# Kernel optimization log

Measured on AMD Instinct MI355X. Metric: run time of the kernel, lower is better.

## Reference

```python
import jax, jax.numpy as jnp
import numpy as np

N = 50000          # nodes
E = 1600000        # edges (avg degree 32)
B = 64             # graphs in batch
D_NODE = 128
D_EDGE = 64
D_EMB = 128
D_HID = 2 * D_EMB  # GCN output channels
EPS = 1e-5


def setup_inputs() -> dict:
    key = jax.random.key(0)
    ks = jax.random.split(key, 12)
    g = lambda k, shape: jax.random.normal(k, shape, jnp.float32) * (shape[0] ** -0.5)
    return {
        "x": jax.random.normal(ks[0], (N, D_NODE), jnp.float32),
        "edge_attr": jax.random.normal(ks[1], (E, D_EDGE), jnp.float32),
        "edge_index": jax.random.randint(ks[2], (2, E), 0, N),
        "batch": jnp.sort(jax.random.randint(ks[3], (N,), 0, B)),
        # GCNConv params
        "W1": g(ks[4], (D_NODE, D_HID)), "b1": jnp.zeros((D_HID,), jnp.float32),
        # TransformerConv params (heads=1)
        "Wq": g(ks[5], (D_HID, D_EMB)), "bq": jnp.zeros((D_EMB,), jnp.float32),
        "Wk": g(ks[6], (D_HID, D_EMB)), "bk": jnp.zeros((D_EMB,), jnp.float32),
        "Wv": g(ks[7], (D_HID, D_EMB)), "bv": jnp.zeros((D_EMB,), jnp.float32),
        "We": g(ks[8], (D_EDGE, D_EMB)), "be": jnp.zeros((D_EMB,), jnp.float32),
        "Wr": g(ks[9], (D_HID, D_EMB)), "br": jnp.zeros((D_EMB,), jnp.float32),
        # LayerNorm params
        "gamma": jnp.ones((D_EMB,), jnp.float32), "beta": jnp.zeros((D_EMB,), jnp.float32),
    }


def _forward(x, edge_attr, edge_index, batch,
             W1, b1, Wq, bq, Wk, bk, Wv, bv, We, be, Wr, br, gamma, beta):
    src, dst = edge_index[0], edge_index[1]

    # ---- GCNConv: symmetric normalization with self-loops ----
    xw = x @ W1                                                # [N, D_HID]
    deg = 1.0 + jax.ops.segment_sum(jnp.ones((E,), x.dtype), dst, num_segments=N)
    dinv = jax.lax.rsqrt(deg)                                  # deg >= 1
    norm = dinv[src] * dinv[dst]                               # [E]
    agg = jax.ops.segment_sum(xw[src] * norm[:, None], dst, num_segments=N)
    h = agg + xw * (dinv * dinv)[:, None] + b1                 # self-loop term
    h = jax.nn.relu(h)                                         # dropout = identity (eval)

    # ---- TransformerConv (heads=1, edge_dim) ----
    q = h @ Wq + bq                                            # [N, D_EMB]
    k = h @ Wk + bk
    v = h @ Wv + bv
    e = edge_attr @ We + be                                    # [E, D_EMB]
    k_j = k[src] + e
    v_j = v[src] + e
    logits = jnp.sum(q[dst] * k_j, axis=-1) / jnp.sqrt(jnp.float32(D_EMB))  # [E]
    # segment softmax over incoming edges of each target node
    lmax = jax.ops.segment_max(logits, dst, num_segments=N)
    exp_l = jnp.exp(logits - lmax[dst])
    denom = jax.ops.segment_sum(exp_l, dst, num_segments=N)
    alpha = exp_l / denom[dst]                                 # [E]
    out = jax.ops.segment_sum(alpha[:, None] * v_j, dst, num_segments=N)
    out = out + h @ Wr + br                                    # root/skip connection

    # ---- LayerNorm + ReLU ----
    mu = jnp.mean(out, axis=-1, keepdims=True)
    var = jnp.var(out, axis=-1, keepdims=True)
    out = (out - mu) * jax.lax.rsqrt(var + EPS) * gamma + beta
    out = jax.nn.relu(out)

    # ---- global mean pool over graphs ----
    sums = jax.ops.segment_sum(out, batch, num_segments=B)     # [B, D_EMB]
    cnts = jax.ops.segment_sum(jnp.ones((N,), out.dtype), batch, num_segments=B)
    return sums / jnp.maximum(cnts, 1.0)[:, None]


def reference(x, edge_attr, edge_index, batch,
              W1, b1, Wq, bq, Wk, bk, Wv, bv, We, be, Wr, br, gamma, beta):
    return _forward(x, edge_attr, edge_index, batch,
                    W1, b1, Wq, bq, Wk, bk, Wv, bv, We, be, Wr, br, gamma, beta)
```

## Files before the change

### kernel.cpp

```cpp
#include <hip/hip_runtime.h>

typedef short bf16x8 __attribute__((ext_vector_type(8)));
typedef float f32x4 __attribute__((ext_vector_type(4)));

#define DN 128
#define DE 64
#define DEMB 128
#define DHID 256
#define SCALE 0.08838834764831845f

__device__ __forceinline__ ushort f2bf(float f) {
  unsigned u = __float_as_uint(f);
  return (ushort)((u + 0x7FFFu + ((u >> 16) & 1u)) >> 16);
}
__device__ __forceinline__ float bf2f(ushort u) {
  return __uint_as_float((unsigned)u << 16);
}

__global__ void k_prep_all(const float* __restrict__ W1, const float* __restrict__ Wq,
                           const float* __restrict__ Wk, const float* __restrict__ Wv,
                           const float* __restrict__ Wr, const float* __restrict__ We,
                           const float* __restrict__ bq, const float* __restrict__ bk,
                           const float* __restrict__ bv, const float* __restrict__ br,
                           const float* __restrict__ be,
// ... 49 lines not shown

__global__ void k_deg(const int* __restrict__ ei, int* __restrict__ degi, int nE) {
  int e = blockIdx.x * 256 + threadIdx.x;
  if (e < nE) atomicAdd(&degi[ei[nE + e]], 1);
}

__global__ __launch_bounds__(1024) void k_scan(const int* __restrict__ degi,
                                               int* __restrict__ row_ptr,
                                               float* __restrict__ dinv, int n) {
  __shared__ int wsum[16];
  __shared__ int carry_s;
  int lane = threadIdx.x & 63, wid = threadIdx.x >> 6;
  if (threadIdx.x == 0) carry_s = 0;
  __syncthreads();
  for (int base = 0; base < n; base += 1024) {
    int i = base + threadIdx.x;
    int v = (i < n) ? degi[i] : 0;
    if (i < n) dinv[i] = rsqrtf(1.0f + (float)v);
    int sc = v;
    #pragma unroll
    for (int off = 1; off < 64; off <<= 1) {
      int t = __shfl_up(sc, off);
      if (lane >= off) sc += t;
    }
    if (lane == 63) wsum[wid] = sc;
    int carry0 = carry_s;
    __syncthreads();
    if (wid == 0) {
      int w = (lane < 16) ? wsum[lane] : 0;
      int swc = w;
      #pragma unroll
      for (int off = 1; off < 16; off <<= 1) {
        int t = __shfl_up(swc, off);
        if (lane >= off) swc += t;
      }
      if (lane < 16) wsum[lane] = swc - w;
      if (lane == 15) carry_s = carry0 + swc;
    }
    __syncthreads();
    if (i < n) row_ptr[i] = carry0 + wsum[wid] + sc - v;
    __syncthreads();
  }
  if (threadIdx.x == 0) row_ptr[n] = carry_s;
}

__global__ void k_scatter(const int* __restrict__ ei, const int* __restrict__ row_ptr,
                          int* __restrict__ cursor, int2* __restrict__ csr_se, int nE) {
  int e = blockIdx.x * 256 + threadIdx.x;
  if (e >= nE) return;
  int dst = ei[nE + e];
  int pos = row_ptr[dst] + atomicAdd(&cursor[dst], 1);
  csr_se[pos] = make_int2(ei[e], e);
}

__global__ __launch_bounds__(256) void k_xcast(const float* __restrict__ x,
                                               const float* __restrict__ dinv,
                                               const int* __restrict__ batch,
                                               int* __restrict__ gstart,
                                               ushort* __restrict__ xsb, int nN, int B) {
  int idx = blockIdx.x * 256 + threadIdx.x;
  if (idx < nN) {
    int b = batch[idx];
    if (idx == 0) {
      for (int g = 0; g <= b; ++g) gstart[g] = 0;
    } else {
      int pb = batch[idx - 1];
      for (int g = pb + 1; g <= b; ++g) gstart[g] = idx;
    }
    if (idx == nN - 1) {
      for (int g = b + 1; g <= B; ++g) gstart[g] = nN;
    }
  }
  if (idx < nN * 32) {
    int n = idx >> 5, q = idx & 31;
    float dn = dinv[n];
    float4 v = *(const float4*)&x[(size_t)n * DN + q * 4];
    ushort4 o;
    o.x = f2bf(v.x * dn); o.y = f2bf(v.y * dn);
    o.z = f2bf(v.z * dn); o.w = f2bf(v.w * dn);
    *(ushort4*)&xsb[(size_t)n * DN + q * 4] = o;
  }
}

__global__ __launch_bounds__(256) void k_gcnX(const ushort* __restrict__ xsb,
                                              const int2* __restrict__ csr_se,
                                              const int* __restrict__ row_ptr,
                                              const float* __restrict__ dinv,
                                              ushort* __restrict__ aggxb, int nN) {
  int lane = threadIdx.x & 63;
  int n = blockIdx.x * 4 + (threadIdx.x >> 6);
  if (n >= nN) return;
  int grp = lane >> 4, l15 = lane & 15;
  int beg = row_ptr[n], end = row_ptr[n + 1];
  float acc[8] = {};

#define GLOAD(S0, S1, X0, X1, base)                                        \
  {                                                                        \
    int e0 = (base) + grp,     c0 = e0 < end ? e0 : end - 1;               \
    int e1 = (base) + 4 + grp, c1 = e1 < end ? e1 : end - 1;               \
    S0 = csr_se[c0].x; S1 = csr_se[c1].x;                                  \
    X0 = *(const uint4*)&xsb[(size_t)S0 * DN + l15 * 8];                   \
    X1 = *(const uint4*)&xsb[(size_t)S1 * DN + l15 * 8];                   \
  }
#define GCOMP(X0, X1, base)                                                \
  {                                                                        \
    float m0 = ((base) + grp < end) ? 1.f : 0.f;                           \
    float m1 = ((base) + 4 + grp < end) ? 1.f : 0.f;                       \
    unsigned q0[4] = {X0.x, X0.y, X0.z, X0.w};                             \
    unsigned q1[4] = {X1.x, X1.y, X1.z, X1.w};                             \
    _Pragma("unroll") for (int d = 0; d < 4; ++d) {                        \
      acc[2*d]   = fmaf(m0, __uint_as_float(q0[d] << 16), acc[2*d]);       \
      acc[2*d+1] = fmaf(m0, __uint_as_float(q0[d] & 0xFFFF0000u), acc[2*d+1]); \
      acc[2*d]   = fmaf(m1, __uint_as_float(q1[d] << 16), acc[2*d]);       \
      acc[2*d+1] = fmaf(m1, __uint_as_float(q1[d] & 0xFFFF0000u), acc[2*d+1]); \
    }                                                                      \
  }

  if (beg < end) {
    int sA0, sA1, sB0, sB1;
    uint4 xA0, xA1, xB0, xB1;
    int i0 = beg;
    GLOAD(sA0, sA1, xA0, xA1, i0);
    while (true) {
      int i1 = i0 + 8;
      if (i1 < end) GLOAD(sB0, sB1, xB0, xB1, i1);
      GCOMP(xA0, xA1, i0);
      i0 = i1;
      if (i0 >= end) break;
      int i2 = i0 + 8;
      if (i2 < end) GLOAD(sA0, sA1, xA0, xA1, i2);
      GCOMP(xB0, xB1, i0);
      i0 = i2;
      if (i0 >= end) break;
    }
  }
#undef GLOAD
#undef GCOMP

  #pragma unroll
  for (int d = 0; d < 8; ++d) {
    acc[d] += __shfl_xor(acc[d], 16);
    acc[d] += __shfl_xor(acc[d], 32);
  }
  if (grp == 0) {
    uint4 sa = *(const uint4*)&xsb[(size_t)n * DN + l15 * 8];
    unsigned sq[4] = {sa.x, sa.y, sa.z, sa.w};
    float dn = dinv[n];
    ushort o[8];
    #pragma unroll
    for (int d = 0; d < 4; ++d) {
      float lo = __uint_as_float(sq[d] << 16);
      float hi = __uint_as_float(sq[d] & 0xFFFF0000u);
      o[2*d]   = f2bf(dn * (acc[2*d]   + lo));
      o[2*d+1] = f2bf(dn * (acc[2*d+1] + hi));
    }
    uint4 ov = {(unsigned)o[0] | ((unsigned)o[1] << 16),
                (unsigned)o[2] | ((unsigned)o[3] << 16),
                (unsigned)o[4] | ((unsigned)o[5] << 16),
                (unsigned)o[6] | ((unsigned)o[7] << 16)};
    *(uint4*)&aggxb[(size_t)n * DN + l15 * 8] = ov;
  }
}

__global__ __launch_bounds__(256) void k_gemm1b(const ushort* __restrict__ aggxb,
                                                const ushort* __restrict__ Wp1,
                                                const float* __restrict__ b1,
                                                ushort* __restrict__ hb, int nN) {
  int lane = threadIdx.x & 63, wave = threadIdx.x >> 6;
  int l15 = lane & 15, lh = lane >> 4;
  int m0 = blockIdx.x * 16;
  int rowa = m0 + l15; if (rowa >= nN) rowa = nN - 1;
  f32x4 acc[4] = {};
  #pragma unroll
  for (int s = 0; s < 4; ++s) {
    bf16x8 af = *(const bf16x8*)&aggxb[(size_t)rowa * DN + s * 32 + lh * 8];
    #pragma unroll
    for (int tt = 0; tt < 4; ++tt) {
      int t = wave * 4 + tt;
      bf16x8 bf = *(const bf16x8*)&Wp1[((t * 4 + s) * 64 + lane) * 8];
      acc[tt] = __builtin_amdgcn_mfma_f32_16x16x32_bf16(af, bf, acc[tt], 0, 0, 0);
    }
  }
  #pragma unroll
  for (int tt = 0; tt < 4; ++tt) {
    int c = (wave * 4 + tt) * 16 + l15;
    float bc = b1[c];
    #pragma unroll
    for (int r = 0; r < 4; ++r) {
      int row = m0 + lh * 4 + r;
      if (row < nN) hb[(size_t)row * DHID + c] = f2bf(fmaxf(acc[tt][r] + bc, 0.f));
    }
  }
}

__global__ __launch_bounds__(256) void k_gemm2(const ushort* __restrict__ hb,
                                               const ushort* __restrict__ Wp2,
                                               const float* __restrict__ bcat,
                                               ushort* __restrict__ qwb,
                                               ushort* __restrict__ kvb,
                                               ushort* __restrict__ hrb, int nN) {
  int lane = threadIdx.x & 63, wave = threadIdx.x >> 6;
  int l15 = lane & 15, lh = lane >> 4;
  int m0 = blockIdx.x * 16;
  int rowa = m0 + l15; if (rowa >= nN) rowa = nN - 1;
  f32x4 acc[9] = {};
  for (int s = 0; s < 8; ++s) {
    bf16x8 af = *(const bf16x8*)&hb[(size_t)rowa * DHID + s * 32 + lh * 8];
    #pragma unroll
    for (int tt = 0; tt < 9; ++tt) {
      int t = wave * 9 + tt;
      bf16x8 bf = *(const bf16x8*)&Wp2[((t * 8 + s) * 64 + lane) * 8];
      acc[tt] = __builtin_amdgcn_mfma_f32_16x16x32_bf16(af, bf, acc[tt], 0, 0, 0);
    }
  }
  #pragma unroll
  for (int tt = 0; tt < 9; ++tt) {
    int c = (wave * 9 + tt) * 16 + l15;
    float bc = bcat[c];
    #pragma unroll
    for (int r = 0; r < 4; ++r) {
      int row = m0 + lh * 4 + r;
      if (row >= nN) continue;
      ushort val = f2bf(acc[tt][r] + bc);
      if (c < 128)      qwb[(size_t)row * 192 + c] = val;
      else if (c < 256) { int d = c - 128; kvb[(size_t)row * 256 + (d >> 3) * 16 + (d & 7)] = val; }
      else if (c < 384) { int d = c - 256; kvb[(size_t)row * 256 + (d >> 3) * 16 + 8 + (d & 7)] = val; }
      else if (c < 512) hrb[(size_t)row * 128 + (c - 384)] = val;
      else              qwb[(size_t)row * 192 + 128 + (c - 512)] = val;
    }
  }
}

__global__ __launch_bounds__(256) void k_edge(const ushort* __restrict__ qwb,
                                              const ushort* __restrict__ kvb,
                                              const float* __restrict__ ea32,
                                              const int2* __restrict__ csr_se,
                                              const int* __restrict__ row_ptr,
                                              float* __restrict__ sden,
                                              float* __restrict__ vaccf,
                                              ushort* __restrict__ ewb, int nN) {
  int lane = threadIdx.x & 63;
  int n = blockIdx.x * 4 + (threadIdx.x >> 6);
  if (n >= nN) return;
  int grp = lane >> 4, l15 = lane & 15;
  const ushort* qp = &qwb[(size_t)n * 192];
  bf16x8 qv = *(const bf16x8*)&qp[l15 * 8];
  ushort4 wv = *(const ushort4*)&qp[128 + l15 * 4];
  float q[8];
  #pragma unroll
  for (int d = 0; d < 8; ++d) q[d] = bf2f((ushort)qv[d]);
  float w0 = bf2f(wv.x), w1 = bf2f(wv.y), w2 = bf2f(wv.z), w3 = bf2f(wv.w);
  float s_acc = 0.f;
  float av[8] = {};
  float ae[4] = {};
  int beg = row_ptr[n], end = row_ptr[n + 1];

#define ELOAD(SE0, SE1, K0, K1, V0, V1, E0, E1, base)                      \
  {                                                                        \
    int e0 = (base) + grp,     c0 = e0 < end ? e0 : end - 1;               \
    int e1 = (base) + 4 + grp, c1 = e1 < end ? e1 : end - 1;               \
    SE0 = csr_se[c0]; SE1 = csr_se[c1];                                    \
    const ushort* r0 = &kvb[(size_t)SE0.x * 256 + l15 * 16];               \
    const ushort* r1 = &kvb[(size_t)SE1.x * 256 + l15 * 16];               \
    K0 = *(const bf16x8*)r0;  V0 = *(const bf16x8*)(r0 + 8);               \
    K1 = *(const bf16x8*)r1;  V1 = *(const bf16x8*)(r1 + 8);               \
    E0 = *(const float4*)&ea32[(size_t)SE0.y * DE + l15 * 4];              \
    E1 = *(const float4*)&ea32[(size_t)SE1.y * DE + l15 * 4];              \
  }
#define ESLOT(K, V, E, valid)                                              \
  {                                                                        \
    float dot = w0 * E.x + w1 * E.y + w2 * E.z + w3 * E.w;                 \
    _Pragma("unroll") for (int d = 0; d < 8; ++d)                          \
      dot = fmaf(q[d], bf2f((ushort)K[d]), dot);                           \
    dot += __shfl_xor(dot, 1);                                             \
    dot += __shfl_xor(dot, 2);                                             \
    dot += __shfl_xor(dot, 4);                                             \
    dot += __shfl_xor(dot, 8);                                             \
    float p = (valid) ? __expf(dot) : 0.f;                                 \
    s_acc += p;                                                            \
    _Pragma("unroll") for (int d = 0; d < 8; ++d)                          \
      av[d] = fmaf(p, bf2f((ushort)V[d]), av[d]);                          \
    ae[0] = fmaf(p, E.x, ae[0]); ae[1] = fmaf(p, E.y, ae[1]);              \
    ae[2] = fmaf(p, E.z, ae[2]); ae[3] = fmaf(p, E.w, ae[3]);              \
  }
#define ECOMP(K0, K1, V0, V1, E0, E1, base)                                \
  {                                                                        \
    ESLOT(K0, V0, E0, (base) + grp < end);                                 \
    ESLOT(K1, V1, E1, (base) + 4 + grp < end);                             \
  }

  if (beg < end) {
    int2 seA0, seA1, seB0, seB1;
    bf16x8 kA0, kA1, vA0, vA1, kB0, kB1, vB0, vB1;
    float4 eA0, eA1, eB0, eB1;
    int i0 = beg;
    ELOAD(seA0, seA1, kA0, kA1, vA0, vA1, eA0, eA1, i0);
    while (true) {
      int i1 = i0 + 8;
      if (i1 < end) ELOAD(seB0, seB1, kB0, kB1, vB0, vB1, eB0, eB1, i1);
      ECOMP(kA0, kA1, vA0, vA1, eA0, eA1, i0);
      i0 = i1;
      if (i0 >= end) break;
      int i2 = i0 + 8;
      if (i2 < end) ELOAD(seA0, seA1, kA0, kA1, vA0, vA1, eA0, eA1, i2);
      ECOMP(kB0, kB1, vB0, vB1, eB0, eB1, i0);
      i0 = i2;
      if (i0 >= end) break;
    }
  }
#undef ELOAD
#undef ESLOT
#undef ECOMP

  s_acc += __shfl_xor(s_acc, 16); s_acc += __shfl_xor(s_acc, 32);
  #pragma unroll
  for (int d = 0; d < 8; ++d) {
    av[d] += __shfl_xor(av[d], 16);
    av[d] += __shfl_xor(av[d], 32);
  }
  #pragma unroll
  for (int d = 0; d < 4; ++d) {
    ae[d] += __shfl_xor(ae[d], 16);
    ae[d] += __shfl_xor(ae[d], 32);
  }
  if (grp == 0) {
    if (l15 == 0) sden[n] = s_acc;
    float4 o0 = {av[0], av[1], av[2], av[3]};
    float4 o1 = {av[4], av[5], av[6], av[7]};
    float* vr = &vaccf[(size_t)n * 128 + l15 * 8];
    *(float4*)vr = o0;
    *(float4*)(vr + 4) = o1;
    ushort4 eo;
    eo.x = f2bf(ae[0]); eo.y = f2bf(ae[1]); eo.z = f2bf(ae[2]); eo.w = f2bf(ae[3]);
    *(ushort4*)&ewb[(size_t)n * DE + l15 * 4] = eo;
  }
}

__global__ __launch_bounds__(256) void k_ewe(const ushort* __restrict__ ewb,
                                             const ushort* __restrict__ Wp3,
                                             float* __restrict__ ewout, int nN) {
  int lane = threadIdx.x & 63, wave = threadIdx.x >> 6;
  int l15 = lane & 15, lh = lane >> 4;
  int m0 = blockIdx.x * 16;
  int rowa = m0 + l15; if (rowa >= nN) rowa = nN - 1;
  f32x4 acc[2] = {};
  #pragma unroll
  for (int s = 0; s < 2; ++s) {
    bf16x8 af = *(const bf16x8*)&ewb[(size_t)rowa * DE + s * 32 + lh * 8];
    #pragma unroll
    for (int tt = 0; tt < 2; ++tt) {
      int t = wave * 2 + tt;
      bf16x8 bf = *(const bf16x8*)&Wp3[((t * 2 + s) * 64 + lane) * 8];
      acc[tt] = __builtin_amdgcn_mfma_f32_16x16x32_bf16(af, bf, acc[tt], 0, 0, 0);
    }
  }
  #pragma unroll
  for (int tt = 0; tt < 2; ++tt) {
    int c = (wave * 2 + tt) * 16 + l15;
    #pragma unroll
    for (int r = 0; r < 4; ++r) {
      int row = m0 + lh * 4 + r;
      if (row < nN) ewout[(size_t)row * 128 + c] = acc[tt][r];
    }
  }
}

__global__ __launch_bounds__(256) void k_fin(const float* __restrict__ sden,
                                             const float* __restrict__ vaccf,
                                             const float* __restrict__ ewout,
                                             const ushort* __restrict__ hrb,
                                             const float* __restrict__ gamma,
                                             const float* __restrict__ beta,
                                             float* __restrict__ ynorm, int nN) {
  int lane = threadIdx.x & 63, grp = lane >> 5, l5 = lane & 31;
  int n = blockIdx.x * 8 + (threadIdx.x >> 6) * 2 + grp;
  if (n >= nN) return;
  float s = sden[n];
  float inv = (s > 0.f) ? 1.f / s : 0.f;
  float4 v4 = *(const float4*)&vaccf[(size_t)n * 128 + l5 * 4];
  float4 w4 = *(const float4*)&ewout[(size_t)n * 128 + l5 * 4];
  ushort4 hv = *(const ushort4*)&hrb[(size_t)n * 128 + l5 * 4];
  float4 o4;
  o4.x = (v4.x + w4.x) * inv + bf2f(hv.x);
  o4.y = (v4.y + w4.y) * inv + bf2f(hv.y);
  o4.z = (v4.z + w4.z) * inv + bf2f(hv.z);
  o4.w = (v4.w + w4.w) * inv + bf2f(hv.w);
  float s1 = o4.x + o4.y + o4.z + o4.w;
  float sq = o4.x*o4.x + o4.y*o4.y + o4.z*o4.z + o4.w*o4.w;
  #pragma unroll
  for (int off = 1; off < 32; off <<= 1) {
    s1 += __shfl_xor(s1, off);
    sq += __shfl_xor(sq, off);
  }
  float mu = s1 * (1.f / 128.f);
  float var = sq * (1.f / 128.f) - mu * mu;
  float rstd = rsqrtf(var + 1e-5f);
  float4 g4 = *(const float4*)&gamma[l5 * 4];
  float4 b4 = *(const float4*)&beta[l5 * 4];
  float4 y;
  y.x = fmaxf((o4.x - mu) * rstd * g4.x + b4.x, 0.f);
  y.y = fmaxf((o4.y - mu) * rstd * g4.y + b4.y, 0.f);
  y.z = fmaxf((o4.z - mu) * rstd * g4.z + b4.z, 0.f);
  y.w = fmaxf((o4.w - mu) * rstd * g4.w + b4.w, 0.f);
  *(float4*)&ynorm[(size_t)n * 128 + l5 * 4] = y;
}

__global__ __launch_bounds__(128) void k_pool(const float* __restrict__ ynorm,
                                              const int* __restrict__ gstart,
                                              float* __restrict__ out) {
  int b = blockIdx.x, t = threadIdx.x;
  int beg = gstart[b], end = gstart[b + 1];
  float a0 = 0.f, a1 = 0.f, a2 = 0.f, a3 = 0.f;
  int n = beg;
  for (; n + 4 <= end; n += 4) {
    a0 += ynorm[(size_t)(n + 0) * 128 + t];
    a1 += ynorm[(size_t)(n + 1) * 128 + t];
    a2 += ynorm[(size_t)(n + 2) * 128 + t];
    a3 += ynorm[(size_t)(n + 3) * 128 + t];
  }
  for (; n < end; ++n) a0 += ynorm[(size_t)n * 128 + t];
  float acc = (a0 + a1) + (a2 + a3);
  out[b * 128 + t] = acc / fmaxf((float)(end - beg), 1.f);
}

extern "C" void kernel_launch(void* const* d_in, const int* in_sizes, int n_in,
                              void* d_out, int out_size, void* d_ws, size_t ws_size,
                              hipStream_t stream) {
  const float* x         = (const float*)d_in[0];
  const float* edge_attr = (const float*)d_in[1];
  const int*   edge_index= (const int*)d_in[2];
  const int*   batch     = (const int*)d_in[3];
  const float* W1 = (const float*)d_in[4];
  const float* b1 = (const float*)d_in[5];
  const float* Wq = (const float*)d_in[6];  const float* bq = (const float*)d_in[7];
  const float* Wk = (const float*)d_in[8];  const float* bk = (const float*)d_in[9];
  const float* Wv = (const float*)d_in[10]; const float* bv = (const float*)d_in[11];
  const float* We = (const float*)d_in[12]; const float* be = (const float*)d_in[13];
  const float* Wr = (const float*)d_in[14]; const float* br = (const float*)d_in[15];
  const float* gamma = (const float*)d_in[16];
  const float* beta  = (const float*)d_in[17];
  float* out = (float*)d_out;

  const int nN = in_sizes[0] / DN;
  const int nE = in_sizes[1] / DE;
  const int B  = out_size / DEMB;

  char* p = (char*)d_ws;
  auto alloc = [&](size_t bytes) -> void* {
    void* r = (void*)p;
    p += (bytes + 255) & ~(size_t)255;
    return r;
  };
  int*   degi   = (int*)  alloc((size_t)nN * 4);
  int*   cursor = (int*)  alloc((size_t)nN * 4);
  size_t zero_bytes = (size_t)(p - (char*)d_ws);
  int*    row_ptr = (int*)   alloc((size_t)(nN + 1) * 4);
  int*    gstart  = (int*)   alloc((size_t)(B + 1) * 4);
  float*  dinv    = (float*) alloc((size_t)nN * 4);
  int2*   csr_se  = (int2*)  alloc((size_t)nE * 8);
  ushort* Wp1     = (ushort*)alloc((size_t)16 * 4 * 64 * 8 * 2);
  ushort* Wp2     = (ushort*)alloc((size_t)36 * 8 * 64 * 8 * 2);
  ushort* Wp3     = (ushort*)alloc((size_t)8 * 2 * 64 * 8 * 2);
  float*  bcat    = (float*) alloc(576 * 4);
  ushort* qwb     = (ushort*)alloc((size_t)nN * 192 * 2);
  ushort* hrb     = (ushort*)alloc((size_t)nN * 128 * 2);
  ushort* hb      = (ushort*)alloc((size_t)nN * DHID * 2);
  ushort* xsb     = (ushort*)alloc((size_t)nN * DN * 2);
  ushort* aggxb   = (ushort*)alloc((size_t)nN * DN * 2);
  ushort* kvb     = xsb;
  float*  sden    = (float*) alloc((size_t)nN * 4);
  float*  vaccf   = (float*) alloc((size_t)nN * 128 * 4);
  ushort* ewb     = (ushort*)alloc((size_t)nN * DE * 2);
  float*  ewout   = (float*) alloc((size_t)nN * 128 * 4);
  float*  ynorm   = (float*) alloc((size_t)nN * 128 * 4);
  size_t required = (size_t)(p - (char*)d_ws);
  if (ws_size < required) return;

  hipMemsetAsync(d_ws, 0, zero_bytes, stream);

  k_prep_all<<<739, 256, 0, stream>>>(W1, Wq, Wk, Wv, Wr, We, bq, bk, bv, br, be,
                                      Wp1, Wp2, Wp3, bcat);
  k_deg<<<(nE + 255) / 256, 256, 0, stream>>>(edge_index, degi, nE);
  k_scan<<<1, 1024, 0, stream>>>(degi, row_ptr, dinv, nN);
  k_scatter<<<(nE + 255) / 256, 256, 0, stream>>>(edge_index, row_ptr, cursor,
                                                  csr_se, nE);
  k_xcast<<<(nN * 32 + 255) / 256, 256, 0, stream>>>(x, dinv, batch, gstart, xsb,
                                                     nN, B);
  k_gcnX<<<(nN + 3) / 4, 256, 0, stream>>>(xsb, csr_se, row_ptr, dinv, aggxb, nN);
  k_gemm1b<<<(nN + 15) / 16, 256, 0, stream>>>(aggxb, Wp1, b1, hb, nN);
  k_gemm2<<<(nN + 15) / 16, 256, 0, stream>>>(hb, Wp2, bcat, qwb, kvb, hrb, nN);
  k_edge<<<(nN + 3) / 4, 256, 0, stream>>>(qwb, kvb, edge_attr, csr_se, row_ptr,
                                           sden, vaccf, ewb, nN);
  k_ewe<<<(nN + 15) / 16, 256, 0, stream>>>(ewb, Wp3, ewout, nN);
  k_fin<<<(nN + 7) / 8, 256, 0, stream>>>(sden, vaccf, ewout, hrb, gamma, beta,
                                          ynorm, nN);
  k_pool<<<B, 128, 0, stream>>>(ynorm, gstart, out);
}
```

Baseline: 616.8 us.

## Fuse GEMM1 into GEMM2 and edge-GEMM into LayerNorm, deepen gather prefetch

Merges the two dense GEMM kernels so the ReLU hidden activations stay in LDS instead of round-tripping through global memory. Merges the edge-feature projection GEMM with the final normalize/LayerNorm kernel, which removes the ewout buffer. Both gather kernels (GCN aggregation and attention edge loop) move from double to triple-buffered register prefetch and get a launch_bounds occupancy hint. kvb gets its own buffer instead of aliasing xsb. In exchange the gather kernels use more registers, and the fused kernels need LDS plus a block barrier.

```diff
diff --git a/kernel.cpp b/kernel.cpp
--- a/kernel.cpp
+++ b/kernel.cpp
@@ -155,11 +155,11 @@
   }
 }
 
-__global__ __launch_bounds__(256) void k_gcnX(const ushort* __restrict__ xsb,
-                                              const int2* __restrict__ csr_se,
-                                              const int* __restrict__ row_ptr,
-                                              const float* __restrict__ dinv,
-                                              ushort* __restrict__ aggxb, int nN) {
+__global__ __launch_bounds__(256, 4) void k_gcnX(const ushort* __restrict__ xsb,
+                                                 const int2* __restrict__ csr_se,
+                                                 const int* __restrict__ row_ptr,
+                                                 const float* __restrict__ dinv,
+                                                 ushort* __restrict__ aggxb, int nN) {
   int lane = threadIdx.x & 63;
   int n = blockIdx.x * 4 + (threadIdx.x >> 6);
   if (n >= nN) return;
@@ -167,13 +167,13 @@
   int beg = row_ptr[n], end = row_ptr[n + 1];
   float acc[8] = {};
 
-#define GLOAD(S0, S1, X0, X1, base)                                        \
+#define GLOAD(X0, X1, base)                                                \
   {                                                                        \
     int e0 = (base) + grp,     c0 = e0 < end ? e0 : end - 1;               \
     int e1 = (base) + 4 + grp, c1 = e1 < end ? e1 : end - 1;               \
-    S0 = csr_se[c0].x; S1 = csr_se[c1].x;                                  \
-    X0 = *(const uint4*)&xsb[(size_t)S0 * DN + l15 * 8];                   \
-    X1 = *(const uint4*)&xsb[(size_t)S1 * DN + l15 * 8];                   \
+    int s0 = csr_se[c0].x, s1 = csr_se[c1].x;                              \
+    X0 = *(const uint4*)&xsb[(size_t)s0 * DN + l15 * 8];                   \
+    X1 = *(const uint4*)&xsb[(size_t)s1 * DN + l15 * 8];                   \
   }
 #define GCOMP(X0, X1, base)                                                \
   {                                                                        \
@@ -190,21 +190,23 @@
   }
 
   if (beg < end) {
-    int sA0, sA1, sB0, sB1;
-    uint4 xA0, xA1, xB0, xB1;
-    int i0 = beg;
-    GLOAD(sA0, sA1, xA0, xA1, i0);
+    uint4 xA0, xA1, xB0, xB1, xC0, xC1;
+    int iA = beg, iB = beg + 8, iC = beg + 16;
+    GLOAD(xA0, xA1, iA);
+    if (iB < end) GLOAD(xB0, xB1, iB);
     while (true) {
-      int i1 = i0 + 8;
-      if (i1 < end) GLOAD(sB0, sB1, xB0, xB1, i1);
-      GCOMP(xA0, xA1, i0);
-      i0 = i1;
-      if (i0 >= end) break;
-      int i2 = i0 + 8;
-      if (i2 < end) GLOAD(sA0, sA1, xA0, xA1, i2);
-      GCOMP(xB0, xB1, i0);
-      i0 = i2;
-      if (i0 >= end) break;
+      if (iC < end) GLOAD(xC0, xC1, iC);
+      GCOMP(xA0, xA1, iA);
+      iA = iC + 8;
+      if (iB >= end) break;
+      if (iA < end) GLOAD(xA0, xA1, iA);
+      GCOMP(xB0, xB1, iB);
+      iB = iA + 8;
+      if (iC >= end) break;
+      if (iB < end) GLOAD(xB0, xB1, iB);
+      GCOMP(xC0, xC1, iC);
+      iC = iB + 8;
+      if (iA >= end) break;
     }
   }
 #undef GLOAD
@@ -235,83 +237,79 @@
   }
 }
 
-__global__ __launch_bounds__(256) void k_gemm1b(const ushort* __restrict__ aggxb,
+__global__ __launch_bounds__(256) void k_gemm12(const ushort* __restrict__ aggxb,
                                                 const ushort* __restrict__ Wp1,
                                                 const float* __restrict__ b1,
-                                                ushort* __restrict__ hb, int nN) {
+                                                const ushort* __restrict__ Wp2,
+                                                const float* __restrict__ bcat,
+                                                ushort* __restrict__ qwb,
+                                                ushort* __restrict__ kvb,
+                                                ushort* __restrict__ hrb, int nN) {
+  __shared__ ushort hlds[16][264];
   int lane = threadIdx.x & 63, wave = threadIdx.x >> 6;
   int l15 = lane & 15, lh = lane >> 4;
   int m0 = blockIdx.x * 16;
   int rowa = m0 + l15; if (rowa >= nN) rowa = nN - 1;
-  f32x4 acc[4] = {};
-  #pragma unroll
-  for (int s = 0; s < 4; ++s) {
-    bf16x8 af = *(const bf16x8*)&aggxb[(size_t)rowa * DN + s * 32 + lh * 8];
+  {
+    f32x4 acc[4] = {};
+    #pragma unroll
+    for (int s = 0; s < 4; ++s) {
+      bf16x8 af = *(const bf16x8*)&aggxb[(size_t)rowa * DN + s * 32 + lh * 8];
+      #pragma unroll
+      for (int tt = 0; tt < 4; ++tt) {
+        int t = wave * 4 + tt;
+        bf16x8 bf = *(const bf16x8*)&Wp1[((t * 4 + s) * 64 + lane) * 8];
+        acc[tt] = __builtin_amdgcn_mfma_f32_16x16x32_bf16(af, bf, acc[tt], 0, 0, 0);
+      }
+    }
     #pragma unroll
     for (int tt = 0; tt < 4; ++tt) {
-      int t = wave * 4 + tt;
-      bf16x8 bf = *(const bf16x8*)&Wp1[((t * 4 + s) * 64 + lane) * 8];
-      acc[tt] = __builtin_amdgcn_mfma_f32_16x16x32_bf16(af, bf, acc[tt], 0, 0, 0);
-    }
-  }
-  #pragma unroll
-  for (int tt = 0; tt < 4; ++tt) {
-    int c = (wave * 4 + tt) * 16 + l15;
-    float bc = b1[c];
-    #pragma unroll
-    for (int r = 0; r < 4; ++r) {
-      int row = m0 + lh * 4 + r;
-      if (row < nN) hb[(size_t)row * DHID + c] = f2bf(fmaxf(acc[tt][r] + bc, 0.f));
-    }
-  }
-}
-
-__global__ __launch_bounds__(256) void k_gemm2(const ushort* __restrict__ hb,
-                                               const ushort* __restrict__ Wp2,
-                                               const float* __restrict__ bcat,
-                                               ushort* __restrict__ qwb,
-                                               ushort* __restrict__ kvb,
-                                               ushort* __restrict__ hrb, int nN) {
-  int lane = threadIdx.x & 63, wave = threadIdx.x >> 6;
-  int l15 = lane & 15, lh = lane >> 4;
-  int m0 = blockIdx.x * 16;
-  int rowa = m0 + l15; if (rowa >= nN) rowa = nN - 1;
-  f32x4 acc[9] = {};
-  for (int s = 0; s < 8; ++s) {
-    bf16x8 af = *(const bf16x8*)&hb[(size_t)rowa * DHID + s * 32 + lh * 8];
+      int c = (wave * 4 + tt) * 16 + l15;
+      float bc = b1[c];
+      #pragma unroll
+      for (int r = 0; r < 4; ++r)
+        hlds[lh * 4 + r][c] = f2bf(fmaxf(acc[tt][r] + bc, 0.f));
+    }
+  }
+  __syncthreads();
+  {
+    f32x4 acc[9] = {};
+    for (int s = 0; s < 8; ++s) {
+      bf16x8 af = *(const bf16x8*)&hlds[l15][s * 32 + lh * 8];
+      #pragma unroll
+      for (int tt = 0; tt < 9; ++tt) {
+        int t = wave * 9 + tt;
+        bf16x8 bf = *(const bf16x8*)&Wp2[((t * 8 + s) * 64 + lane) * 8];
+        acc[tt] = __builtin_amdgcn_mfma_f32_16x16x32_bf16(af, bf, acc[tt], 0, 0, 0);
+      }
+    }
     #pragma unroll
     for (int tt = 0; tt < 9; ++tt) {
-      int t = wave * 9 + tt;
-      bf16x8 bf = *(const bf16x8*)&Wp2[((t * 8 + s) * 64 + lane) * 8];
-      acc[tt] = __builtin_amdgcn_mfma_f32_16x16x32_bf16(af, bf, acc[tt], 0, 0, 0);
-    }
-  }
-  #pragma unroll
-  for (int tt = 0; tt < 9; ++tt) {
-    int c = (wave * 9 + tt) * 16 + l15;
-    float bc = bcat[c];
-    #pragma unroll
-    for (int r = 0; r < 4; ++r) {
-      int row = m0 + lh * 4 + r;
-      if (row >= nN) continue;
-      ushort val = f2bf(acc[tt][r] + bc);
-      if (c < 128)      qwb[(size_t)row * 192 + c] = val;
-      else if (c < 256) { int d = c - 128; kvb[(size_t)row * 256 + (d >> 3) * 16 + (d & 7)] = val; }
-      else if (c < 384) { int d = c - 256; kvb[(size_t)row * 256 + (d >> 3) * 16 + 8 + (d & 7)] = val; }
-      else if (c < 512) hrb[(size_t)row * 128 + (c - 384)] = val;
-      else              qwb[(size_t)row * 192 + 128 + (c - 512)] = val;
-    }
-  }
-}
-
-__global__ __launch_bounds__(256) void k_edge(const ushort* __restrict__ qwb,
-                                              const ushort* __restrict__ kvb,
-                                              const float* __restrict__ ea32,
-                                              const int2* __restrict__ csr_se,
-                                              const int* __restrict__ row_ptr,
-                                              float* __restrict__ sden,
-                                              float* __restrict__ vaccf,
-                                              ushort* __restrict__ ewb, int nN) {
+      int c = (wave * 9 + tt) * 16 + l15;
+      float bc = bcat[c];
+      #pragma unroll
+      for (int r = 0; r < 4; ++r) {
+        int row = m0 + lh * 4 + r;
+        if (row >= nN) continue;
+        ushort val = f2bf(acc[tt][r] + bc);
+        if (c < 128)      qwb[(size_t)row * 192 + c] = val;
+        else if (c < 256) { int d = c - 128; kvb[(size_t)row * 256 + (d >> 3) * 16 + (d & 7)] = val; }
+        else if (c < 384) { int d = c - 256; kvb[(size_t)row * 256 + (d >> 3) * 16 + 8 + (d & 7)] = val; }
+        else if (c < 512) hrb[(size_t)row * 128 + (c - 384)] = val;
+        else              qwb[(size_t)row * 192 + 128 + (c - 512)] = val;
+      }
+    }
+  }
+}
+
+__global__ __launch_bounds__(256, 4) void k_edge(const ushort* __restrict__ qwb,
+                                                 const ushort* __restrict__ kvb,
+                                                 const float* __restrict__ ea32,
+                                                 const int2* __restrict__ csr_se,
+                                                 const int* __restrict__ row_ptr,
+                                                 float* __restrict__ sden,
+                                                 float* __restrict__ vaccf,
+                                                 ushort* __restrict__ ewb, int nN) {
   int lane = threadIdx.x & 63;
   int n = blockIdx.x * 4 + (threadIdx.x >> 6);
   if (n >= nN) return;
@@ -328,17 +326,17 @@
   float ae[4] = {};
   int beg = row_ptr[n], end = row_ptr[n + 1];
 
-#define ELOAD(SE0, SE1, K0, K1, V0, V1, E0, E1, base)                      \
+#define ELOAD(K0, K1, V0, V1, E0, E1, base)                                \
   {                                                                        \
     int e0 = (base) + grp,     c0 = e0 < end ? e0 : end - 1;               \
     int e1 = (base) + 4 + grp, c1 = e1 < end ? e1 : end - 1;               \
-    SE0 = csr_se[c0]; SE1 = csr_se[c1];                                    \
-    const ushort* r0 = &kvb[(size_t)SE0.x * 256 + l15 * 16];               \
-    const ushort* r1 = &kvb[(size_t)SE1.x * 256 + l15 * 16];               \
+    int2 se0 = csr_se[c0], se1 = csr_se[c1];                               \
+    const ushort* r0 = &kvb[(size_t)se0.x * 256 + l15 * 16];               \
+    const ushort* r1 = &kvb[(size_t)se1.x * 256 + l15 * 16];               \
     K0 = *(const bf16x8*)r0;  V0 = *(const bf16x8*)(r0 + 8);               \
     K1 = *(const bf16x8*)r1;  V1 = *(const bf16x8*)(r1 + 8);               \
-    E0 = *(const float4*)&ea32[(size_t)SE0.y * DE + l15 * 4];              \
-    E1 = *(const float4*)&ea32[(size_t)SE1.y * DE + l15 * 4];              \
+    E0 = *(const float4*)&ea32[(size_t)se0.y * DE + l15 * 4];              \
+    E1 = *(const float4*)&ea32[(size_t)se1.y * DE + l15 * 4];              \
   }
 #define ESLOT(K, V, E, valid)                                              \
   {                                                                        \
@@ -363,22 +361,24 @@
   }
 
   if (beg < end) {
-    int2 seA0, seA1, seB0, seB1;
-    bf16x8 kA0, kA1, vA0, vA1, kB0, kB1, vB0, vB1;
-    float4 eA0, eA1, eB0, eB1;
-    int i0 = beg;
-    ELOAD(seA0, seA1, kA0, kA1, vA0, vA1, eA0, eA1, i0);
+    bf16x8 kA0, kA1, vA0, vA1, kB0, kB1, vB0, vB1, kC0, kC1, vC0, vC1;
+    float4 eA0, eA1, eB0, eB1, eC0, eC1;
+    int iA = beg, iB = beg + 8, iC = beg + 16;
+    ELOAD(kA0, kA1, vA0, vA1, eA0, eA1, iA);
+    if (iB < end) ELOAD(kB0, kB1, vB0, vB1, eB0, eB1, iB);
     while (true) {
-      int i1 = i0 + 8;
-      if (i1 < end) ELOAD(seB0, seB1, kB0, kB1, vB0, vB1, eB0, eB1, i1);
-      ECOMP(kA0, kA1, vA0, vA1, eA0, eA1, i0);
-      i0 = i1;
-      if (i0 >= end) break;
-      int i2 = i0 + 8;
-      if (i2 < end) ELOAD(seA0, seA1, kA0, kA1, vA0, vA1, eA0, eA1, i2);
-      ECOMP(kB0, kB1, vB0, vB1, eB0, eB1, i0);
-      i0 = i2;
-      if (i0 >= end) break;
+      if (iC < end) ELOAD(kC0, kC1, vC0, vC1, eC0, eC1, iC);
+      ECOMP(kA0, kA1, vA0, vA1, eA0, eA1, iA);
+      iA = iC + 8;
+      if (iB >= end) break;
+      if (iA < end) ELOAD(kA0, kA1, vA0, vA1, eA0, eA1, iA);
+      ECOMP(kB0, kB1, vB0, vB1, eB0, eB1, iB);
+      iB = iA + 8;
+      if (iC >= end) break;
+      if (iB < end) ELOAD(kB0, kB1, vB0, vB1, eB0, eB1, iB);
+      ECOMP(kC0, kC1, vC0, vC1, eC0, eC1, iC);
+      iC = iB + 8;
+      if (iA >= end) break;
     }
   }
 #undef ELOAD
@@ -409,73 +409,74 @@
   }
 }
 
-__global__ __launch_bounds__(256) void k_ewe(const ushort* __restrict__ ewb,
-                                             const ushort* __restrict__ Wp3,
-                                             float* __restrict__ ewout, int nN) {
+__global__ __launch_bounds__(256) void k_ewefin(const ushort* __restrict__ ewb,
+                                                const ushort* __restrict__ Wp3,
+                                                const float* __restrict__ sden,
+                                                const float* __restrict__ vaccf,
+                                                const ushort* __restrict__ hrb,
+                                                const float* __restrict__ gamma,
+                                                const float* __restrict__ beta,
+                                                float* __restrict__ ynorm, int nN) {
+  __shared__ float elds[16][132];
   int lane = threadIdx.x & 63, wave = threadIdx.x >> 6;
   int l15 = lane & 15, lh = lane >> 4;
   int m0 = blockIdx.x * 16;
-  int rowa = m0 + l15; if (rowa >= nN) rowa = nN - 1;
-  f32x4 acc[2] = {};
+  {
+    int rowa = m0 + l15; if (rowa >= nN) rowa = nN - 1;
+    f32x4 acc[2] = {};
+    #pragma unroll
+    for (int s = 0; s < 2; ++s) {
+      bf16x8 af = *(const bf16x8*)&ewb[(size_t)rowa * DE + s * 32 + lh * 8];
+      #pragma unroll
+      for (int tt = 0; tt < 2; ++tt) {
+        int t = wave * 2 + tt;
+        bf16x8 bf = *(const bf16x8*)&Wp3[((t * 2 + s) * 64 + lane) * 8];
+        acc[tt] = __builtin_amdgcn_mfma_f32_16x16x32_bf16(af, bf, acc[tt], 0, 0, 0);
+      }
+    }
+    #pragma unroll
+    for (int tt = 0; tt < 2; ++tt) {
+      int c = (wave * 2 + tt) * 16 + l15;
+      #pragma unroll
+      for (int r = 0; r < 4; ++r) elds[lh * 4 + r][c] = acc[tt][r];
+    }
+  }
+  __syncthreads();
+  int grp = lane >> 5, l5 = lane & 31;
   #pragma unroll
-  for (int s = 0; s < 2; ++s) {
-    bf16x8 af = *(const bf16x8*)&ewb[(size_t)rowa * DE + s * 32 + lh * 8];
-    #pragma unroll
-    for (int tt = 0; tt < 2; ++tt) {
-      int t = wave * 2 + tt;
-      bf16x8 bf = *(const bf16x8*)&Wp3[((t * 2 + s) * 64 + lane) * 8];
-      acc[tt] = __builtin_amdgcn_mfma_f32_16x16x32_bf16(af, bf, acc[tt], 0, 0, 0);
-    }
-  }
-  #pragma unroll
-  for (int tt = 0; tt < 2; ++tt) {
-    int c = (wave * 2 + tt) * 16 + l15;
-    #pragma unroll
-    for (int r = 0; r < 4; ++r) {
-      int row = m0 + lh * 4 + r;
-      if (row < nN) ewout[(size_t)row * 128 + c] = acc[tt][r];
-    }
-  }
-}
-
-__global__ __launch_bounds__(256) void k_fin(const float* __restrict__ sden,
-                                             const float* __restrict__ vaccf,
-                                             const float* __restrict__ ewout,
-                                             const ushort* __restrict__ hrb,
-                                             const float* __restrict__ gamma,
-                                             const float* __restrict__ beta,
-                                             float* __restrict__ ynorm, int nN) {
-  int lane = threadIdx.x & 63, grp = lane >> 5, l5 = lane & 31;
-  int n = blockIdx.x * 8 + (threadIdx.x >> 6) * 2 + grp;
-  if (n >= nN) return;
-  float s = sden[n];
-  float inv = (s > 0.f) ? 1.f / s : 0.f;
-  float4 v4 = *(const float4*)&vaccf[(size_t)n * 128 + l5 * 4];
-  float4 w4 = *(const float4*)&ewout[(size_t)n * 128 + l5 * 4];
-  ushort4 hv = *(const ushort4*)&hrb[(size_t)n * 128 + l5 * 4];
-  float4 o4;
-  o4.x = (v4.x + w4.x) * inv + bf2f(hv.x);
-  o4.y = (v4.y + w4.y) * inv + bf2f(hv.y);
-  o4.z = (v4.z + w4.z) * inv + bf2f(hv.z);
-  o4.w = (v4.w + w4.w) * inv + bf2f(hv.w);
-  float s1 = o4.x + o4.y + o4.z + o4.w;
-  float sq = o4.x*o4.x + o4.y*o4.y + o4.z*o4.z + o4.w*o4.w;
-  #pragma unroll
-  for (int off = 1; off < 32; off <<= 1) {
-    s1 += __shfl_xor(s1, off);
-    sq += __shfl_xor(sq, off);
-  }
-  float mu = s1 * (1.f / 128.f);
-  float var = sq * (1.f / 128.f) - mu * mu;
-  float rstd = rsqrtf(var + 1e-5f);
-  float4 g4 = *(const float4*)&gamma[l5 * 4];
-  float4 b4 = *(const float4*)&beta[l5 * 4];
-  float4 y;
-  y.x = fmaxf((o4.x - mu) * rstd * g4.x + b4.x, 0.f);
-  y.y = fmaxf((o4.y - mu) * rstd * g4.y + b4.y, 0.f);
-  y.z = fmaxf((o4.z - mu) * rstd * g4.z + b4.z, 0.f);
-  y.w = fmaxf((o4.w - mu) * rstd * g4.w + b4.w, 0.f);
-  *(float4*)&ynorm[(size_t)n * 128 + l5 * 4] = y;
+  for (int rr = 0; rr < 2; ++rr) {
+    int rl = wave * 4 + rr * 2 + grp;
+    int n = m0 + rl;
+    if (n >= nN) continue;
+    float s = sden[n];
+    float inv = (s > 0.f) ? 1.f / s : 0.f;
+    float4 v4 = *(const float4*)&vaccf[(size_t)n * 128 + l5 * 4];
+    float4 w4 = *(const float4*)&elds[rl][l5 * 4];
+    ushort4 hv = *(const ushort4*)&hrb[(size_t)n * 128 + l5 * 4];
+    float4 o4;
+    o4.x = (v4.x + w4.x) * inv + bf2f(hv.x);
+    o4.y = (v4.y + w4.y) * inv + bf2f(hv.y);
+    o4.z = (v4.z + w4.z) * inv + bf2f(hv.z);
+    o4.w = (v4.w + w4.w) * inv + bf2f(hv.w);
+    float s1 = o4.x + o4.y + o4.z + o4.w;
+    float sq = o4.x*o4.x + o4.y*o4.y + o4.z*o4.z + o4.w*o4.w;
+    #pragma unroll
+    for (int off = 1; off < 32; off <<= 1) {
+      s1 += __shfl_xor(s1, off);
+      sq += __shfl_xor(sq, off);
+    }
+    float mu = s1 * (1.f / 128.f);
+    float var = sq * (1.f / 128.f) - mu * mu;
+    float rstd = rsqrtf(var + 1e-5f);
+    float4 g4 = *(const float4*)&gamma[l5 * 4];
+    float4 b4 = *(const float4*)&beta[l5 * 4];
+    float4 y;
+    y.x = fmaxf((o4.x - mu) * rstd * g4.x + b4.x, 0.f);
+    y.y = fmaxf((o4.y - mu) * rstd * g4.y + b4.y, 0.f);
+    y.z = fmaxf((o4.z - mu) * rstd * g4.z + b4.z, 0.f);
+    y.w = fmaxf((o4.w - mu) * rstd * g4.w + b4.w, 0.f);
+    *(float4*)&ynorm[(size_t)n * 128 + l5 * 4] = y;
+  }
 }
 
 __global__ __launch_bounds__(128) void k_pool(const float* __restrict__ ynorm,
@@ -537,14 +538,12 @@
   float*  bcat    = (float*) alloc(576 * 4);
   ushort* qwb     = (ushort*)alloc((size_t)nN * 192 * 2);
   ushort* hrb     = (ushort*)alloc((size_t)nN * 128 * 2);
-  ushort* hb      = (ushort*)alloc((size_t)nN * DHID * 2);
   ushort* xsb     = (ushort*)alloc((size_t)nN * DN * 2);
   ushort* aggxb   = (ushort*)alloc((size_t)nN * DN * 2);
-  ushort* kvb     = xsb;
+  ushort* kvb     = (ushort*)alloc((size_t)nN * 256 * 2);
   float*  sden    = (float*) alloc((size_t)nN * 4);
   float*  vaccf   = (float*) alloc((size_t)nN * 128 * 4);
   ushort* ewb     = (ushort*)alloc((size_t)nN * DE * 2);
-  float*  ewout   = (float*) alloc((size_t)nN * 128 * 4);
   float*  ynorm   = (float*) alloc((size_t)nN * 128 * 4);
   size_t required = (size_t)(p - (char*)d_ws);
   if (ws_size < required) return;
@@ -560,12 +559,11 @@
   k_xcast<<<(nN * 32 + 255) / 256, 256, 0, stream>>>(x, dinv, batch, gstart, xsb,
                                                      nN, B);
   k_gcnX<<<(nN + 3) / 4, 256, 0, stream>>>(xsb, csr_se, row_ptr, dinv, aggxb, nN);
-  k_gemm1b<<<(nN + 15) / 16, 256, 0, stream>>>(aggxb, Wp1, b1, hb, nN);
-  k_gemm2<<<(nN + 15) / 16, 256, 0, stream>>>(hb, Wp2, bcat, qwb, kvb, hrb, nN);
+  k_gemm12<<<(nN + 15) / 16, 256, 0, stream>>>(aggxb, Wp1, b1, Wp2, bcat,
+                                               qwb, kvb, hrb, nN);
   k_edge<<<(nN + 3) / 4, 256, 0, stream>>>(qwb, kvb, edge_attr, csr_se, row_ptr,
                                            sden, vaccf, ewb, nN);
-  k_ewe<<<(nN + 15) / 16, 256, 0, stream>>>(ewb, Wp3, ewout, nN);
-  k_fin<<<(nN + 7) / 8, 256, 0, stream>>>(sden, vaccf, ewout, hrb, gamma, beta,
-                                          ynorm, nN);
+  k_ewefin<<<(nN + 15) / 16, 256, 0, stream>>>(ewb, Wp3, sden, vaccf, hrb,
+                                               gamma, beta, ynorm, nN);
   k_pool<<<B, 128, 0, stream>>>(ynorm, gstart, out);
 }
```

After: 827.0 us. 1.34x slower.

## Fuse GEMM1 into GEMM2 and edge-weight GEMM into LayerNorm finalize via LDS

Applied to the files above, without the earlier changes.

Merges the GCN output GEMM with the Q/K/V/root projection GEMM so each 16-row tile of the hidden activations stays in shared memory instead of being written to and read back from a global buffer. It also merges the edge-feature projection GEMM with the normalization/LayerNorm finalize kernel, keeping the 128-wide edge term in LDS instead of a float32 global buffer. This removes two kernel launches and two intermediate global round-trips. In exchange, kvb gets its own allocation instead of aliasing xsb, and the workspace layout changes. The fused kernels also add a block barrier and LDS usage, which may reduce occupancy.

```diff
diff --git a/kernel.cpp b/kernel.cpp
--- a/kernel.cpp
+++ b/kernel.cpp
@@ -235,71 +235,67 @@
   }
 }
 
-__global__ __launch_bounds__(256) void k_gemm1b(const ushort* __restrict__ aggxb,
+__global__ __launch_bounds__(256) void k_gemm12(const ushort* __restrict__ aggxb,
                                                 const ushort* __restrict__ Wp1,
                                                 const float* __restrict__ b1,
-                                                ushort* __restrict__ hb, int nN) {
+                                                const ushort* __restrict__ Wp2,
+                                                const float* __restrict__ bcat,
+                                                ushort* __restrict__ qwb,
+                                                ushort* __restrict__ kvb,
+                                                ushort* __restrict__ hrb, int nN) {
+  __shared__ ushort hlds[16][264];
   int lane = threadIdx.x & 63, wave = threadIdx.x >> 6;
   int l15 = lane & 15, lh = lane >> 4;
   int m0 = blockIdx.x * 16;
   int rowa = m0 + l15; if (rowa >= nN) rowa = nN - 1;
-  f32x4 acc[4] = {};
-  #pragma unroll
-  for (int s = 0; s < 4; ++s) {
-    bf16x8 af = *(const bf16x8*)&aggxb[(size_t)rowa * DN + s * 32 + lh * 8];
+  {
+    f32x4 acc[4] = {};
+    #pragma unroll
+    for (int s = 0; s < 4; ++s) {
+      bf16x8 af = *(const bf16x8*)&aggxb[(size_t)rowa * DN + s * 32 + lh * 8];
+      #pragma unroll
+      for (int tt = 0; tt < 4; ++tt) {
+        int t = wave * 4 + tt;
+        bf16x8 bf = *(const bf16x8*)&Wp1[((t * 4 + s) * 64 + lane) * 8];
+        acc[tt] = __builtin_amdgcn_mfma_f32_16x16x32_bf16(af, bf, acc[tt], 0, 0, 0);
+      }
+    }
     #pragma unroll
     for (int tt = 0; tt < 4; ++tt) {
-      int t = wave * 4 + tt;
-      bf16x8 bf = *(const bf16x8*)&Wp1[((t * 4 + s) * 64 + lane) * 8];
-      acc[tt] = __builtin_amdgcn_mfma_f32_16x16x32_bf16(af, bf, acc[tt], 0, 0, 0);
-    }
-  }
-  #pragma unroll
-  for (int tt = 0; tt < 4; ++tt) {
-    int c = (wave * 4 + tt) * 16 + l15;
-    float bc = b1[c];
-    #pragma unroll
-    for (int r = 0; r < 4; ++r) {
-      int row = m0 + lh * 4 + r;
-      if (row < nN) hb[(size_t)row * DHID + c] = f2bf(fmaxf(acc[tt][r] + bc, 0.f));
-    }
-  }
-}
-
-__global__ __launch_bounds__(256) void k_gemm2(const ushort* __restrict__ hb,
-                                               const ushort* __restrict__ Wp2,
-                                               const float* __restrict__ bcat,
-                                               ushort* __restrict__ qwb,
-                                               ushort* __restrict__ kvb,
-                                               ushort* __restrict__ hrb, int nN) {
-  int lane = threadIdx.x & 63, wave = threadIdx.x >> 6;
-  int l15 = lane & 15, lh = lane >> 4;
-  int m0 = blockIdx.x * 16;
-  int rowa = m0 + l15; if (rowa >= nN) rowa = nN - 1;
-  f32x4 acc[9] = {};
-  for (int s = 0; s < 8; ++s) {
-    bf16x8 af = *(const bf16x8*)&hb[(size_t)rowa * DHID + s * 32 + lh * 8];
+      int c = (wave * 4 + tt) * 16 + l15;
+      float bc = b1[c];
+      #pragma unroll
+      for (int r = 0; r < 4; ++r)
+        hlds[lh * 4 + r][c] = f2bf(fmaxf(acc[tt][r] + bc, 0.f));
+    }
+  }
+  __syncthreads();
+  {
+    f32x4 acc[9] = {};
+    for (int s = 0; s < 8; ++s) {
+      bf16x8 af = *(const bf16x8*)&hlds[l15][s * 32 + lh * 8];
+      #pragma unroll
+      for (int tt = 0; tt < 9; ++tt) {
+        int t = wave * 9 + tt;
+        bf16x8 bf = *(const bf16x8*)&Wp2[((t * 8 + s) * 64 + lane) * 8];
+        acc[tt] = __builtin_amdgcn_mfma_f32_16x16x32_bf16(af, bf, acc[tt], 0, 0, 0);
+      }
+    }
     #pragma unroll
     for (int tt = 0; tt < 9; ++tt) {
-      int t = wave * 9 + tt;
-      bf16x8 bf = *(const bf16x8*)&Wp2[((t * 8 + s) * 64 + lane) * 8];
-      acc[tt] = __builtin_amdgcn_mfma_f32_16x16x32_bf16(af, bf, acc[tt], 0, 0, 0);
-    }
-  }
-  #pragma unroll
-  for (int tt = 0; tt < 9; ++tt) {
-    int c = (wave * 9 + tt) * 16 + l15;
-    float bc = bcat[c];
-    #pragma unroll
-    for (int r = 0; r < 4; ++r) {
-      int row = m0 + lh * 4 + r;
-      if (row >= nN) continue;
-      ushort val = f2bf(acc[tt][r] + bc);
-      if (c < 128)      qwb[(size_t)row * 192 + c] = val;
-      else if (c < 256) { int d = c - 128; kvb[(size_t)row * 256 + (d >> 3) * 16 + (d & 7)] = val; }
-      else if (c < 384) { int d = c - 256; kvb[(size_t)row * 256 + (d >> 3) * 16 + 8 + (d & 7)] = val; }
-      else if (c < 512) hrb[(size_t)row * 128 + (c - 384)] = val;
-      else              qwb[(size_t)row * 192 + 128 + (c - 512)] = val;
+      int c = (wave * 9 + tt) * 16 + l15;
+      float bc = bcat[c];
+      #pragma unroll
+      for (int r = 0; r < 4; ++r) {
+        int row = m0 + lh * 4 + r;
+        if (row >= nN) continue;
+        ushort val = f2bf(acc[tt][r] + bc);
+        if (c < 128)      qwb[(size_t)row * 192 + c] = val;
+        else if (c < 256) { int d = c - 128; kvb[(size_t)row * 256 + (d >> 3) * 16 + (d & 7)] = val; }
+        else if (c < 384) { int d = c - 256; kvb[(size_t)row * 256 + (d >> 3) * 16 + 8 + (d & 7)] = val; }
+        else if (c < 512) hrb[(size_t)row * 128 + (c - 384)] = val;
+        else              qwb[(size_t)row * 192 + 128 + (c - 512)] = val;
+      }
     }
   }
 }
@@ -409,73 +405,74 @@
   }
 }
 
-__global__ __launch_bounds__(256) void k_ewe(const ushort* __restrict__ ewb,
-                                             const ushort* __restrict__ Wp3,
-                                             float* __restrict__ ewout, int nN) {
+__global__ __launch_bounds__(256) void k_ewefin(const ushort* __restrict__ ewb,
+                                                const ushort* __restrict__ Wp3,
+                                                const float* __restrict__ sden,
+                                                const float* __restrict__ vaccf,
+                                                const ushort* __restrict__ hrb,
+                                                const float* __restrict__ gamma,
+                                                const float* __restrict__ beta,
+                                                float* __restrict__ ynorm, int nN) {
+  __shared__ float elds[16][132];
   int lane = threadIdx.x & 63, wave = threadIdx.x >> 6;
   int l15 = lane & 15, lh = lane >> 4;
   int m0 = blockIdx.x * 16;
-  int rowa = m0 + l15; if (rowa >= nN) rowa = nN - 1;
-  f32x4 acc[2] = {};
+  {
+    int rowa = m0 + l15; if (rowa >= nN) rowa = nN - 1;
+    f32x4 acc[2] = {};
+    #pragma unroll
+    for (int s = 0; s < 2; ++s) {
+      bf16x8 af = *(const bf16x8*)&ewb[(size_t)rowa * DE + s * 32 + lh * 8];
+      #pragma unroll
+      for (int tt = 0; tt < 2; ++tt) {
+        int t = wave * 2 + tt;
+        bf16x8 bf = *(const bf16x8*)&Wp3[((t * 2 + s) * 64 + lane) * 8];
+        acc[tt] = __builtin_amdgcn_mfma_f32_16x16x32_bf16(af, bf, acc[tt], 0, 0, 0);
+      }
+    }
+    #pragma unroll
+    for (int tt = 0; tt < 2; ++tt) {
+      int c = (wave * 2 + tt) * 16 + l15;
+      #pragma unroll
+      for (int r = 0; r < 4; ++r) elds[lh * 4 + r][c] = acc[tt][r];
+    }
+  }
+  __syncthreads();
+  int grp = lane >> 5, l5 = lane & 31;
   #pragma unroll
-  for (int s = 0; s < 2; ++s) {
-    bf16x8 af = *(const bf16x8*)&ewb[(size_t)rowa * DE + s * 32 + lh * 8];
-    #pragma unroll
-    for (int tt = 0; tt < 2; ++tt) {
-      int t = wave * 2 + tt;
-      bf16x8 bf = *(const bf16x8*)&Wp3[((t * 2 + s) * 64 + lane) * 8];
-      acc[tt] = __builtin_amdgcn_mfma_f32_16x16x32_bf16(af, bf, acc[tt], 0, 0, 0);
-    }
-  }
-  #pragma unroll
-  for (int tt = 0; tt < 2; ++tt) {
-    int c = (wave * 2 + tt) * 16 + l15;
-    #pragma unroll
-    for (int r = 0; r < 4; ++r) {
-      int row = m0 + lh * 4 + r;
-      if (row < nN) ewout[(size_t)row * 128 + c] = acc[tt][r];
-    }
-  }
-}
-
-__global__ __launch_bounds__(256) void k_fin(const float* __restrict__ sden,
-                                             const float* __restrict__ vaccf,
-                                             const float* __restrict__ ewout,
-                                             const ushort* __restrict__ hrb,
-                                             const float* __restrict__ gamma,
-                                             const float* __restrict__ beta,
-                                             float* __restrict__ ynorm, int nN) {
-  int lane = threadIdx.x & 63, grp = lane >> 5, l5 = lane & 31;
-  int n = blockIdx.x * 8 + (threadIdx.x >> 6) * 2 + grp;
-  if (n >= nN) return;
-  float s = sden[n];
-  float inv = (s > 0.f) ? 1.f / s : 0.f;
-  float4 v4 = *(const float4*)&vaccf[(size_t)n * 128 + l5 * 4];
-  float4 w4 = *(const float4*)&ewout[(size_t)n * 128 + l5 * 4];
-  ushort4 hv = *(const ushort4*)&hrb[(size_t)n * 128 + l5 * 4];
-  float4 o4;
-  o4.x = (v4.x + w4.x) * inv + bf2f(hv.x);
-  o4.y = (v4.y + w4.y) * inv + bf2f(hv.y);
-  o4.z = (v4.z + w4.z) * inv + bf2f(hv.z);
-  o4.w = (v4.w + w4.w) * inv + bf2f(hv.w);
-  float s1 = o4.x + o4.y + o4.z + o4.w;
-  float sq = o4.x*o4.x + o4.y*o4.y + o4.z*o4.z + o4.w*o4.w;
-  #pragma unroll
-  for (int off = 1; off < 32; off <<= 1) {
-    s1 += __shfl_xor(s1, off);
-    sq += __shfl_xor(sq, off);
-  }
-  float mu = s1 * (1.f / 128.f);
-  float var = sq * (1.f / 128.f) - mu * mu;
-  float rstd = rsqrtf(var + 1e-5f);
-  float4 g4 = *(const float4*)&gamma[l5 * 4];
-  float4 b4 = *(const float4*)&beta[l5 * 4];
-  float4 y;
-  y.x = fmaxf((o4.x - mu) * rstd * g4.x + b4.x, 0.f);
-  y.y = fmaxf((o4.y - mu) * rstd * g4.y + b4.y, 0.f);
-  y.z = fmaxf((o4.z - mu) * rstd * g4.z + b4.z, 0.f);
-  y.w = fmaxf((o4.w - mu) * rstd * g4.w + b4.w, 0.f);
-  *(float4*)&ynorm[(size_t)n * 128 + l5 * 4] = y;
+  for (int rr = 0; rr < 2; ++rr) {
+    int rl = wave * 4 + rr * 2 + grp;
+    int n = m0 + rl;
+    if (n >= nN) continue;
+    float s = sden[n];
+    float inv = (s > 0.f) ? 1.f / s : 0.f;
+    float4 v4 = *(const float4*)&vaccf[(size_t)n * 128 + l5 * 4];
+    float4 w4 = *(const float4*)&elds[rl][l5 * 4];
+    ushort4 hv = *(const ushort4*)&hrb[(size_t)n * 128 + l5 * 4];
+    float4 o4;
+    o4.x = (v4.x + w4.x) * inv + bf2f(hv.x);
+    o4.y = (v4.y + w4.y) * inv + bf2f(hv.y);
+    o4.z = (v4.z + w4.z) * inv + bf2f(hv.z);
+    o4.w = (v4.w + w4.w) * inv + bf2f(hv.w);
+    float s1 = o4.x + o4.y + o4.z + o4.w;
+    float sq = o4.x*o4.x + o4.y*o4.y + o4.z*o4.z + o4.w*o4.w;
+    #pragma unroll
+    for (int off = 1; off < 32; off <<= 1) {
+      s1 += __shfl_xor(s1, off);
+      sq += __shfl_xor(sq, off);
+    }
+    float mu = s1 * (1.f / 128.f);
+    float var = sq * (1.f / 128.f) - mu * mu;
+    float rstd = rsqrtf(var + 1e-5f);
+    float4 g4 = *(const float4*)&gamma[l5 * 4];
+    float4 b4 = *(const float4*)&beta[l5 * 4];
+    float4 y;
+    y.x = fmaxf((o4.x - mu) * rstd * g4.x + b4.x, 0.f);
+    y.y = fmaxf((o4.y - mu) * rstd * g4.y + b4.y, 0.f);
+    y.z = fmaxf((o4.z - mu) * rstd * g4.z + b4.z, 0.f);
+    y.w = fmaxf((o4.w - mu) * rstd * g4.w + b4.w, 0.f);
+    *(float4*)&ynorm[(size_t)n * 128 + l5 * 4] = y;
+  }
 }
 
 __global__ __launch_bounds__(128) void k_pool(const float* __restrict__ ynorm,
@@ -537,14 +534,12 @@
   float*  bcat    = (float*) alloc(576 * 4);
   ushort* qwb     = (ushort*)alloc((size_t)nN * 192 * 2);
   ushort* hrb     = (ushort*)alloc((size_t)nN * 128 * 2);
-  ushort* hb      = (ushort*)alloc((size_t)nN * DHID * 2);
   ushort* xsb     = (ushort*)alloc((size_t)nN * DN * 2);
   ushort* aggxb   = (ushort*)alloc((size_t)nN * DN * 2);
-  ushort* kvb     = xsb;
+  ushort* kvb     = (ushort*)alloc((size_t)nN * 256 * 2);
   float*  sden    = (float*) alloc((size_t)nN * 4);
   float*  vaccf   = (float*) alloc((size_t)nN * 128 * 4);
   ushort* ewb     = (ushort*)alloc((size_t)nN * DE * 2);
-  float*  ewout   = (float*) alloc((size_t)nN * 128 * 4);
   float*  ynorm   = (float*) alloc((size_t)nN * 128 * 4);
   size_t required = (size_t)(p - (char*)d_ws);
   if (ws_size < required) return;
@@ -560,12 +555,11 @@
   k_xcast<<<(nN * 32 + 255) / 256, 256, 0, stream>>>(x, dinv, batch, gstart, xsb,
                                                      nN, B);
   k_gcnX<<<(nN + 3) / 4, 256, 0, stream>>>(xsb, csr_se, row_ptr, dinv, aggxb, nN);
-  k_gemm1b<<<(nN + 15) / 16, 256, 0, stream>>>(aggxb, Wp1, b1, hb, nN);
-  k_gemm2<<<(nN + 15) / 16, 256, 0, stream>>>(hb, Wp2, bcat, qwb, kvb, hrb, nN);
+  k_gemm12<<<(nN + 15) / 16, 256, 0, stream>>>(aggxb, Wp1, b1, Wp2, bcat,
+                                               qwb, kvb, hrb, nN);
   k_edge<<<(nN + 3) / 4, 256, 0, stream>>>(qwb, kvb, edge_attr, csr_se, row_ptr,
                                            sden, vaccf, ewb, nN);
-  k_ewe<<<(nN + 15) / 16, 256, 0, stream>>>(ewb, Wp3, ewout, nN);
-  k_fin<<<(nN + 7) / 8, 256, 0, stream>>>(sden, vaccf, ewout, hrb, gamma, beta,
-                                          ynorm, nN);
+  k_ewefin<<<(nN + 15) / 16, 256, 0, stream>>>(ewb, Wp3, sden, vaccf, hrb,
+                                               gamma, beta, ynorm, nN);
   k_pool<<<B, 128, 0, stream>>>(ynorm, gstart, out);
 }
```

Result: faster. 600.2 us (-2.7%).
